# Performance work log

Measured on AMD Instinct MI355X. Metric: run time of the kernel, lower is better.

Reference implementation:

```python
import jax, jax.numpy as jnp
import numpy as np

B, LQ, D, DFF, NH, DH, NL, NP = 8, 1024, 256, 1024, 8, 32, 3, 4
_SHAPES = np.array([[100, 100], [50, 50], [25, 25]], dtype=np.int32)  # (H, W) per level
_AREAS = _SHAPES[:, 0] * _SHAPES[:, 1]
LIN = int(_AREAS.sum())  # 13125
_STARTS = np.concatenate([[0], np.cumsum(_AREAS)[:-1]]).astype(np.int32)


def setup_inputs() -> dict:
    key = jax.random.key(0)
    ks = iter(jax.random.split(key, 64))
    def rn(shape, s=1.0):
        return jax.random.normal(next(ks), shape, jnp.float32) * s
    return {
        "query_embed": rn((B, LQ, D)),
        "query_mask": jnp.zeros((B, LQ), bool),  # True = padded key
        "query_order": rn((B, LQ, D)),
        "values": rn((B, LIN, D)),
        "ref_point": jax.random.uniform(next(ks), (B, LQ, 2), jnp.float32),
        "ref_pos": rn((B, LQ, D)),
        "ref_feat": rn((B, LQ, D)),
        "shapes": jnp.asarray(_SHAPES),
        "level_start": jnp.asarray(_STARTS),
        "headwise_refpoint_idxs": jnp.zeros((B, LQ), jnp.int32),  # unused (side_head=0)
        # self-attention sub-block params (nn.MultiheadAttention packed in-proj)
        "sa_in_w": rn((D, 3 * D), 0.02), "sa_in_b": jnp.zeros((3 * D,)),
        "sa_out_w": rn((D, D), 0.02), "sa_out_b": jnp.zeros((D,)),
        "sa_ln1_g": jnp.ones((D,)), "sa_ln1_b": jnp.zeros((D,)),
        "sa_l1_w": rn((D, DFF), 0.02), "sa_l1_b": jnp.zeros((DFF,)),
        "sa_l2_w": rn((DFF, D), 0.02), "sa_l2_b": jnp.zeros((D,)),
        "sa_ln2_g": jnp.ones((D,)), "sa_ln2_b": jnp.zeros((D,)),
        # MDeformAttn params
        "da_val_w": rn((D, D), 0.02), "da_val_b": jnp.zeros((D,)),
        "da_off_w": rn((D, NH * NL * NP * 2), 0.001), "da_off_b": rn((NH * NL * NP * 2,), 0.01),
        "da_att_w": rn((D, NH * NL * NP), 0.02), "da_att_b": jnp.zeros((NH * NL * NP,)),
        "da_out_w": rn((D, D), 0.02), "da_out_b": jnp.zeros((D,)),
        # post-deform FFN block params
        "ln1_g": jnp.ones((D,)), "ln1_b": jnp.zeros((D,)),
        "ff1_w": rn((D, DFF), 0.02), "ff1_b": jnp.zeros((DFF,)),
        "ff2_w": rn((DFF, D), 0.02), "ff2_b": jnp.zeros((D,)),
        "ln2_g": jnp.ones((D,)), "ln2_b": jnp.zeros((D,)),
    }


def _ln(x, g, b):
    m = jnp.mean(x, -1, keepdims=True)
    v = jnp.mean((x - m) ** 2, -1, keepdims=True)
    return (x - m) / jnp.sqrt(v + 1e-5) * g + b


def _mha(q, k, v, key_padding_mask, in_w, in_b, out_w, out_b):
    Bv = q.shape[0]
    qp = (q @ in_w[:, :D] + in_b[:D]).reshape(Bv, -1, NH, DH)
    kp = (k @ in_w[:, D:2 * D] + in_b[D:2 * D]).reshape(Bv, -1, NH, DH)
    vp = (v @ in_w[:, 2 * D:] + in_b[2 * D:]).reshape(Bv, -1, NH, DH)
    scores = jnp.einsum('bqhd,bkhd->bhqk', qp, kp) / jnp.sqrt(jnp.float32(DH))
    scores = scores + jnp.where(key_padding_mask[:, None, None, :], -1e9, 0.0)
    a = jax.nn.softmax(scores, -1)
    o = jnp.einsum('bhqk,bkhd->bqhd', a, vp).reshape(Bv, -1, D)
    return o @ out_w + out_b


def _ms_deform(query, ref_point, values, shapes,
               val_w, val_b, off_w, off_b, att_w, att_b, out_w, out_b):
    # Multi-scale deformable attention (MDeformAttn, align_corners=False bilinear, zero pad)
    Bv, Lq = query.shape[0], query.shape[1]
    v = (values @ val_w + val_b).reshape(Bv, -1, NH, DH)
    off = (query @ off_w + off_b).reshape(Bv, Lq, NH, NL, NP, 2)
    attn = jax.nn.softmax((query @ att_w + att_b).reshape(Bv, Lq, NH, NL * NP), -1)
    attn = attn.reshape(Bv, Lq, NH, NL, NP)
    norm = jnp.stack([shapes[:, 1], shapes[:, 0]], -1).astype(jnp.float32)  # (W, H)
    loc = ref_point[:, :, None, None, None, :] + off / norm[None, None, None, :, None, :]
    acc = 0.0
    for lvl in range(NL):  # static spatial shapes per level
        Hl, Wl = int(_SHAPES[lvl, 0]), int(_SHAPES[lvl, 1])
        s = int(_STARTS[lvl])
        vl = v[:, s:s + Hl * Wl].transpose(0, 2, 1, 3)  # [B,NH,Hl*Wl,DH]
        ll = loc[:, :, :, lvl]                          # [B,Lq,NH,NP,2]
        x = ll[..., 0] * Wl - 0.5
        y = ll[..., 1] * Hl - 0.5
        x0 = jnp.floor(x); y0 = jnp.floor(y)
        wx = x - x0; wy = y - y0
        x0i = x0.astype(jnp.int32); y0i = y0.astype(jnp.int32)
        def tw(w):  # [B,Lq,NH,NP] -> [B,NH,Lq*NP,1]
            return w.transpose(0, 2, 1, 3).reshape(Bv, NH, -1, 1)
        def gather(yy, xx):
            valid = ((yy >= 0) & (yy < Hl) & (xx >= 0) & (xx < Wl))
            idx = jnp.clip(yy, 0, Hl - 1) * Wl + jnp.clip(xx, 0, Wl - 1)
            idx_t = idx.transpose(0, 2, 1, 3).reshape(Bv, NH, -1)
            g = jnp.take_along_axis(vl, idx_t[..., None], axis=2)  # [B,NH,Lq*NP,DH]
            return g * tw(valid.astype(vl.dtype))
        samp = (tw((1 - wy) * (1 - wx)) * gather(y0i, x0i)
                + tw((1 - wy) * wx) * gather(y0i, x0i + 1)
                + tw(wy * (1 - wx)) * gather(y0i + 1, x0i)
                + tw(wy * wx) * gather(y0i + 1, x0i + 1))
        aw = tw(attn[:, :, :, lvl])
        acc = acc + (samp * aw).reshape(Bv, NH, Lq, NP, DH).sum(3)
    out = acc.transpose(0, 2, 1, 3).reshape(Bv, Lq, D)
    return out @ out_w + out_b


def reference(query_embed, query_mask, query_order, values, ref_point, ref_pos, ref_feat,
              shapes, level_start, headwise_refpoint_idxs,
              sa_in_w, sa_in_b, sa_out_w, sa_out_b, sa_ln1_g, sa_ln1_b,
              sa_l1_w, sa_l1_b, sa_l2_w, sa_l2_b, sa_ln2_g, sa_ln2_b,
              da_val_w, da_val_b, da_off_w, da_off_b, da_att_w, da_att_b, da_out_w, da_out_b,
              ln1_g, ln1_b, ff1_w, ff1_b, ff2_w, ff2_b, ln2_g, ln2_b):
    # forward_self_att(tgt + ref_feat, query_order + ref_pos, query_mask); dropout = identity (eval)
    src = query_embed + ref_feat
    pos = query_order + ref_pos
    q = src + pos
    src = _ln(src + _mha(q, q, src, query_mask, sa_in_w, sa_in_b, sa_out_w, sa_out_b), sa_ln1_g, sa_ln1_b)
    src = _ln(src + (jax.nn.relu(src @ sa_l1_w + sa_l1_b) @ sa_l2_w + sa_l2_b), sa_ln2_g, sa_ln2_b)
    tgt = src
    dq = tgt + query_order + ref_pos + ref_feat
    tgt2 = _ms_deform(dq, ref_point, values, shapes,
                      da_val_w, da_val_b, da_off_w, da_off_b, da_att_w, da_att_b, da_out_w, da_out_b)
    tgt = _ln(tgt + tgt2, ln1_g, ln1_b)
    tgt = _ln(tgt + (jax.nn.relu(tgt @ ff1_w + ff1_b) @ ff2_w + ff2_b), ln2_g, ln2_b)
    return tgt
```

## Files before the change

### kernel.cpp

```cpp
#include <hip/hip_runtime.h>
#include <math.h>

#define B_   8
#define LQ_  1024
#define D_   256
#define NH_  8
#define DH_  32
#define LIN_ 13125

typedef __attribute__((ext_vector_type(4))) float f32x4;
typedef __attribute__((ext_vector_type(8))) short bf16x8;
typedef __attribute__((ext_vector_type(4))) short bf16x4;

__device__ __forceinline__ float4 f4add(float4 a, float4 b){
  return make_float4(a.x+b.x, a.y+b.y, a.z+b.z, a.w+b.w);
}
__device__ __forceinline__ unsigned short f2bf(float f){
  unsigned u = __float_as_uint(f);
  unsigned r = (u + 0x7fffu + ((u>>16)&1u)) >> 16;
  return (unsigned short)r;
}
__device__ __forceinline__ float bf2f(unsigned short u){
  return __uint_as_float(((unsigned)u)<<16);
}
__device__ __forceinline__ unsigned pk2(float a, float b){
  return (unsigned)f2bf(a) | ((unsigned)f2bf(b)<<16);
}
__device__ __forceinline__ float fexp2(float x){
#if __has_builtin(__builtin_amdgcn_exp2f)
  return __builtin_amdgcn_exp2f(x);
#else
  return exp2f(x);
#endif
}
__device__ __forceinline__ f32x4 mfma16x16(bf16x4 a, bf16x4 b, f32x4 c){
#if __has_builtin(__builtin_amdgcn_mfma_f32_16x16x16_bf16)
  return __builtin_amdgcn_mfma_f32_16x16x16_bf16(a, b, c, 0, 0, 0);
#else
  asm volatile("s_nop 1\n\tv_mfma_f32_16x16x16_bf16 %0, %1, %2, %0"
               : "+v"(c) : "v"(a), "v"(b));
  return c;
#endif
}
__device__ __forceinline__ void gload16(const void* g, void* l){
  __builtin_amdgcn_global_load_lds(
      (const __attribute__((address_space(1))) void*)g,
      (__attribute__((address_space(3))) void*)l, 16, 0, 0);
}
__device__ __forceinline__ bf16x8 cvt8(const float4& a, const float4& b){
  unsigned u0,u1,u2,u3;
  asm("v_cvt_pk_bf16_f32 %0, %1, %2" : "=v"(u0) : "v"(a.x), "v"(a.y));
  asm("v_cvt_pk_bf16_f32 %0, %1, %2" : "=v"(u1) : "v"(a.z), "v"(a.w));
  asm("v_cvt_pk_bf16_f32 %0, %1, %2" : "=v"(u2) : "v"(b.x), "v"(b.y));
  asm("v_cvt_pk_bf16_f32 %0, %1, %2" : "=v"(u3) : "v"(b.z), "v"(b.w));
  uint4 uu = make_uint4(u0,u1,u2,u3);
  return __builtin_bit_cast(bf16x8, uu);
}
__device__ __forceinline__ int xcd_swz(int lin, int nwg){
  if (nwg < 64) return lin;
  const int q = nwg >> 3, r = nwg & 7;
  const int x = lin & 7, d = lin >> 3;
  return (x < r ? x*(q+1) : r*(q+1) + (x-r)*q) + d;
}

__global__ __launch_bounds__(256) void k_prep(
    const float4* __restrict__ qe, const float4* __restrict__ rf,
    const float4* __restrict__ qo, const float4* __restrict__ rp,
    const unsigned char* __restrict__ mask,
    const float* __restrict__ off_b, const float* __restrict__ att_b,
    float4* __restrict__ src, uint2* __restrict__ srcb, uint2* __restrict__ qb,
    float* __restrict__ biasf, float* __restrict__ biasoa)
{
  int i = blockIdx.x*256 + threadIdx.x;
  if (i < B_*LQ_) biasf[i] = mask[i] ? -2.0e9f : 0.f;
  if (blockIdx.x == 32) {
    for (int j = threadIdx.x; j < 384; j += 256)
      biasoa[j] = (j < 192) ? off_b[j] : (j < 288 ? att_b[j-192] : 0.f);
  }
  float4 s = f4add(qe[i], rf[i]);
  src[i] = s;
  float4 q = f4add(s, f4add(qo[i], rp[i]));
  srcb[i] = make_uint2(pk2(s.x,s.y), pk2(s.z,s.w));
  qb[i]   = make_uint2(pk2(q.x,q.y), pk2(q.z,q.w));
}

struct WEnt { const float* s; unsigned short* d; int K; int N; };
struct WPack { WEnt e[10]; };
__global__ __launch_bounds__(256) void k_wtcvt(WPack p)
{
  __shared__ float sm[32][33];
  WEnt w = p.e[blockIdx.y];
  const int tk = w.K >> 5, tn = w.N >> 5;
  const int nt = tk * tn;
  const int r = threadIdx.x >> 5, c = threadIdx.x & 31;
  for (int tile = blockIdx.x; tile < nt; tile += gridDim.x) {
    const int ti = tile / tn, tj = tile % tn;
    #pragma unroll
    for (int rr = r; rr < 32; rr += 8)
      sm[rr][c] = w.s[(size_t)(ti*32+rr)*w.N + tj*32 + c];
    __syncthreads();
    #pragma unroll
    for (int rr = r; rr < 32; rr += 8)
      w.d[(size_t)(tj*32+rr)*w.K + ti*32 + c] = f2bf(sm[c][rr]);
    __syncthreads();
  }
}

template<bool BF16OUT>
__global__ __launch_bounds__(256) void k_gemm_bf(
    const unsigned short* __restrict__ A, int lda,
    const unsigned short* __restrict__ Wt,
    const float* __restrict__ bias,
    float* __restrict__ Cf, unsigned short* __restrict__ Cb, int ldc,
    int M, int N, int K, int relu)
{
  __shared__ unsigned short As[2][4096];
  __shared__ unsigned short Bs[2][4096];
  const int t = threadIdx.x;
  const int lin = xcd_swz(blockIdx.y*gridDim.x + blockIdx.x, gridDim.x*gridDim.y);
  const int bx = lin % gridDim.x, by = lin / gridDim.x;
  const int m0 = by * 128;
  const int n0 = bx * 128;
  const int w  = t >> 6, lane = t & 63;
  const int lr = lane & 15, lg = lane >> 4;
  const int wm = (w & 1) * 64, wn = (w >> 1) * 64;

  const int rowc  = t >> 2;
  const int cbs8  = (((t & 3) ^ ((t >> 2) & 3)) << 3);
  const size_t ra0 = (size_t)min(m0 + rowc,      M-1) * lda;
  const size_t ra1 = (size_t)min(m0 + rowc + 64, M-1) * lda;
  const size_t rb0 = (size_t)(n0 + rowc)      * K;
  const size_t rb1 = (size_t)(n0 + rowc + 64) * K;
  unsigned short* la0[2] = { &As[0][(w<<9)],        &As[1][(w<<9)] };
  unsigned short* la1[2] = { &As[0][2048+(w<<9)],   &As[1][2048+(w<<9)] };
  unsigned short* lb0[2] = { &Bs[0][(w<<9)],        &Bs[1][(w<<9)] };
  unsigned short* lb1[2] = { &Bs[0][2048+(w<<9)],   &Bs[1][2048+(w<<9)] };

  f32x4 acc[4][4];
  #pragma unroll
  for (int i=0;i<4;++i)
    #pragma unroll
    for (int j=0;j<4;++j) acc[i][j] = (f32x4){0.f,0.f,0.f,0.f};

  const int cswz = ((lg ^ (lr & 3)) << 3);
  const int nt = K >> 5;

  {
    gload16(A  + ra0 + cbs8, la0[0]);
    gload16(A  + ra1 + cbs8, la1[0]);
    gload16(Wt + rb0 + cbs8, lb0[0]);
    gload16(Wt + rb1 + cbs8, lb1[0]);
  }
  for (int ks = 0; ks < nt; ++ks) {
    const int cur = ks & 1;
    __syncthreads();
    if (ks + 1 < nt) {
      const int kb = (ks + 1) << 5;
      const int nb = cur ^ 1;
      gload16(A  + ra0 + kb + cbs8, la0[nb]);
      gload16(A  + ra1 + kb + cbs8, la1[nb]);
      gload16(Wt + rb0 + kb + cbs8, lb0[nb]);
      gload16(Wt + rb1 + kb + cbs8, lb1[nb]);
    }
    bf16x8 af[4], bfr[4];
    #pragma unroll
    for (int mi=0;mi<4;++mi)
      af[mi]  = *reinterpret_cast<const bf16x8*>(&As[cur][(wm+mi*16+lr)*32 + cswz]);
    #pragma unroll
    for (int ni=0;ni<4;++ni)
      bfr[ni] = *reinterpret_cast<const bf16x8*>(&Bs[cur][(wn+ni*16+lr)*32 + cswz]);
    #pragma unroll
    for (int mi=0;mi<4;++mi)
      #pragma unroll
      for (int ni=0;ni<4;++ni)
        acc[mi][ni] = __builtin_amdgcn_mfma_f32_16x16x32_bf16(af[mi], bfr[ni], acc[mi][ni], 0, 0, 0);
  }

  float bs[4];
  #pragma unroll
  for (int ni=0;ni<4;++ni) bs[ni] = bias[n0 + wn + ni*16 + lr];
  #pragma unroll
  for (int mi=0;mi<4;++mi){
    #pragma unroll
    for (int i=0;i<4;++i){
      const int row = m0 + wm + mi*16 + lg*4 + i;
      if (row >= M) continue;
      #pragma unroll
      for (int ni=0;ni<4;++ni){
        const int col = n0 + wn + ni*16 + lr;
        float v = acc[mi][ni][i] + bs[ni];
        if (relu) v = fmaxf(v, 0.f);
        if (BF16OUT) Cb[(size_t)row*ldc + col] = f2bf(v);
        else         Cf[(size_t)row*ldc + col] = v;
      }
    }
  }
}

__global__ __launch_bounds__(256, 2) void k_gemm_vp(
    const float* __restrict__ A,
    const unsigned short* __restrict__ Wt,
    const float* __restrict__ bias,
    unsigned short* __restrict__ Cb, int M)
{
  __shared__ unsigned short Ws[32768];
  const int t = threadIdx.x;
  const int lin = xcd_swz(blockIdx.y*gridDim.x + blockIdx.x, gridDim.x*gridDim.y);
  const int bx = lin % gridDim.x, by = lin / gridDim.x;
  const int n0 = bx * 128;
  const int m0 = by * 256;
  const int w = t >> 6, lane = t & 63;
  const int lr = lane & 15, lg = lane >> 4;

  #pragma unroll
  for (int q = 0; q < 16; ++q) {
    const int c = q*256 + t;
    const int row = c >> 5, pos = c & 31;
    gload16(Wt + (size_t)(n0 + row)*256 + ((pos ^ (row & 31)) << 3),
            (unsigned short*)Ws + (size_t)c*8);
  }
  __syncthreads();

  float bs[8];
  #pragma unroll
  for (int ni=0;ni<8;++ni) bs[ni] = bias[n0 + ni*16 + lr];

  const int mw = m0 + w*64;
  float4 avA[8][2], avB[8][2];
  #pragma unroll
  for (int kk=0;kk<8;++kk){
    const size_t ad = (size_t)min(mw + lr, M-1)*256 + kk*32 + lg*8;
    avA[kk][0] = *reinterpret_cast<const float4*>(A + ad);
    avA[kk][1] = *reinterpret_cast<const float4*>(A + ad + 4);
  }
  #pragma unroll
  for (int s = 0; s < 4; ++s) {
    const int mb = mw + s*16;
    if (s < 3) {
      #pragma unroll
      for (int kk=0;kk<8;++kk){
        const size_t ad = (size_t)min(mb + 16 + lr, M-1)*256 + kk*32 + lg*8;
        if (s & 1) {
          avA[kk][0] = *reinterpret_cast<const float4*>(A + ad);
          avA[kk][1] = *reinterpret_cast<const float4*>(A + ad + 4);
        } else {
          avB[kk][0] = *reinterpret_cast<const float4*>(A + ad);
          avB[kk][1] = *reinterpret_cast<const float4*>(A + ad + 4);
        }
      }
    }
    bf16x8 af[8];
    #pragma unroll
    for (int kk=0;kk<8;++kk)
      af[kk] = (s & 1) ? cvt8(avB[kk][0], avB[kk][1]) : cvt8(avA[kk][0], avA[kk][1]);
    f32x4 acc[8];
    #pragma unroll
    for (int ni=0;ni<8;++ni) acc[ni] = (f32x4){0.f,0.f,0.f,0.f};
    #pragma unroll
    for (int kk=0;kk<8;++kk){
      #pragma unroll
      for (int ni=0;ni<8;++ni){
        const int r = ni*16 + lr;
        const int p = (kk*4 + lg) ^ (r & 31);
        bf16x8 wf = *reinterpret_cast<const bf16x8*>(&Ws[r*256 + (p<<3)]);
        acc[ni] = __builtin_amdgcn_mfma_f32_16x16x32_bf16(af[kk], wf, acc[ni], 0, 0, 0);
      }
    }
    #pragma unroll
    for (int ni=0;ni<8;++ni){
      const int col = n0 + ni*16 + lr;
      #pragma unroll
      for (int i=0;i<4;++i){
        const int row = mb + lg*4 + i;
        if (row < M) Cb[(size_t)row*256 + col] = f2bf(acc[ni][i] + bs[ni]);
      }
    }
  }
}

template<int EPI>
__global__ __launch_bounds__(256) void k_gemm64(
    const unsigned short* __restrict__ A, int lda,
    const unsigned short* __restrict__ Wt,
    const float* __restrict__ bias,
    float* __restrict__ Cf, unsigned short* __restrict__ Cb, int ldc,
    int M, int N, int K, int relu)
{
  __shared__ unsigned short As[2][4096];
  __shared__ unsigned short Bs[2][4096];
  const int t = threadIdx.x;
  const int lin = xcd_swz(blockIdx.y*gridDim.x + blockIdx.x, gridDim.x*gridDim.y);
  const int bx = lin % gridDim.x, by = lin / gridDim.x;
  const int m0 = by * 64;
  const int n0 = bx * 64;
  const int w = t >> 6, lane = t & 63;
  const int lr = lane & 15, lg = lane >> 4;
  const int wm = (w & 1) * 32, wn = (w >> 1) * 32;

  const int c0 = w*64 + lane;
  const int c1 = 256 + w*64 + lane;
  const int r0c = c0 >> 3, s0c = ((c0 & 7) ^ (r0c & 7)) << 3;
  const int r1c = c1 >> 3, s1c = ((c1 & 7) ^ (r1c & 7)) << 3;
  const size_t a0 = (size_t)(m0 + r0c)*lda + s0c;
  const size_t a1 = (size_t)(m0 + r1c)*lda + s1c;
  const size_t b0 = (size_t)(n0 + r0c)*K + s0c;
  const size_t b1 = (size_t)(n0 + r1c)*K + s1c;
  const int d0 = w*512, d1 = 2048 + w*512;

  f32x4 acc[2][2];
  acc[0][0]=acc[0][1]=acc[1][0]=acc[1][1]=(f32x4){0.f,0.f,0.f,0.f};

  gload16(A + a0, &As[0][d0]);  gload16(A + a1, &As[0][d1]);
  gload16(Wt + b0, &Bs[0][d0]); gload16(Wt + b1, &Bs[0][d1]);
  const int nt = K >> 6;
  for (int ks = 0; ks < nt; ++ks) {
    const int cur = ks & 1;
    __syncthreads();
    if (ks + 1 < nt) {
      const int kb = (ks + 1) << 6;
      const int nb = cur ^ 1;
      gload16(A + kb + a0, &As[nb][d0]);  gload16(A + kb + a1, &As[nb][d1]);
      gload16(Wt + kb + b0, &Bs[nb][d0]); gload16(Wt + kb + b1, &Bs[nb][d1]);
    }
    bf16x8 af[2][2], bfr[2][2];
    #pragma unroll
    for (int mi=0;mi<2;++mi){
      const int r = wm + mi*16 + lr;
      #pragma unroll
      for (int kk=0;kk<2;++kk){
        const int ch = ((kk*4 + lg) ^ (r & 7)) << 3;
        af[mi][kk] = *reinterpret_cast<const bf16x8*>(&As[cur][r*64 + ch]);
      }
    }
    #pragma unroll
    for (int ni=0;ni<2;++ni){
      const int r = wn + ni*16 + lr;
      #pragma unroll
      for (int kk=0;kk<2;++kk){
        const int ch = ((kk*4 + lg) ^ (r & 7)) << 3;
        bfr[ni][kk] = *reinterpret_cast<const bf16x8*>(&Bs[cur][r*64 + ch]);
      }
    }
    #pragma unroll
    for (int kk=0;kk<2;++kk)
      #pragma unroll
      for (int mi=0;mi<2;++mi)
        #pragma unroll
        for (int ni=0;ni<2;++ni)
          acc[mi][ni] = __builtin_amdgcn_mfma_f32_16x16x32_bf16(af[mi][kk], bfr[ni][kk], acc[mi][ni], 0, 0, 0);
  }

  float bs[2];
  bs[0] = bias[n0 + wn + lr];
  bs[1] = bias[n0 + wn + 16 + lr];
  if (EPI == 3) {
    #pragma unroll
    for (int mi=0;mi<2;++mi){
      const int rowb = m0 + wm + mi*16 + lg*4;
      #pragma unroll
      for (int ni=0;ni<2;++ni){
        const int colb = n0 + wn + ni*16 + lr;
        const int bh = (rowb >> 10)*8 + (colb >> 5);
        const int d = colb & 31;
        ushort4 pkv;
        pkv.x = f2bf(acc[mi][ni][0] + bs[ni]);
        pkv.y = f2bf(acc[mi][ni][1] + bs[ni]);
        pkv.z = f2bf(acc[mi][ni][2] + bs[ni]);
        pkv.w = f2bf(acc[mi][ni][3] + bs[ni]);
        *reinterpret_cast<ushort4*>(Cb + (size_t)bh*32768 + (size_t)d*1024 + (rowb & 1023)) = pkv;
      }
    }
    return;
  }
  #pragma unroll
  for (int mi=0;mi<2;++mi){
    #pragma unroll
    for (int i=0;i<4;++i){
      const int row = m0 + wm + mi*16 + lg*4 + i;
      #pragma unroll
      for (int ni=0;ni<2;++ni){
        const int col = n0 + wn + ni*16 + lr;
        float v = acc[mi][ni][i] + bs[ni];
        if (relu) v = fmaxf(v, 0.f);
        if (EPI == 0) {
          Cf[(size_t)row*ldc + col] = v;
        } else if (EPI == 1) {
          Cb[(size_t)row*ldc + col] = f2bf(v);
        } else {
          const int ch = col & 255;
          const int sel = col >> 8;
          const int bh = (row >> 10)*8 + (ch >> 5);
          Cb[(size_t)sel*2097152 + (size_t)bh*32768 + (size_t)(row & 1023)*32 + (ch & 31)] = f2bf(v);
        }
      }
    }
  }
}

__global__ __launch_bounds__(256) void k_gemm_ln(
    const unsigned short* __restrict__ A, int lda,
    const unsigned short* __restrict__ Wt,
    const float* __restrict__ bias,
    const float* __restrict__ X,
    const float* __restrict__ g, const float* __restrict__ be,
    float* __restrict__ out,
    unsigned short* __restrict__ ab,
    const float* __restrict__ qo, const float* __restrict__ rp,
    const float* __restrict__ rf, unsigned short* __restrict__ dqb,
    int K)
{
  __shared__ unsigned short As[2][1024];
  __shared__ unsigned short Bs[2][16384];
  __shared__ float part[4][16][2];
  const int t = threadIdx.x;
  const int w = t >> 6, lane = t & 63;
  const int lr = lane & 15, lg = lane >> 4;
  const int m0 = xcd_swz(blockIdx.x, gridDim.x) * 16;

  const int ar = t >> 3, ac = t & 7;
  const size_t aSrc = (size_t)(m0 + ar)*lda + ((ac ^ (ar & 7)) << 3);
  size_t bSrc[8];
  #pragma unroll
  for (int q=0;q<8;++q){
    const int c = q*256 + t;
    const int br = c >> 3, bc = c & 7;
    bSrc[q] = (size_t)br*K + ((bc ^ (br & 7)) << 3);
  }

  f32x4 acc[4];
  #pragma unroll
  for (int ni=0;ni<4;++ni) acc[ni] = (f32x4){0.f,0.f,0.f,0.f};

  if (w < 2) gload16(A + aSrc, &As[0][(w<<9)]);
  #pragma unroll
  for (int q=0;q<8;++q) gload16(Wt + bSrc[q], &Bs[0][q*2048 + (w<<9)]);

  const int nt = K >> 6;
  for (int ks = 0; ks < nt; ++ks) {
    const int cur = ks & 1;
    __syncthreads();
    if (ks + 1 < nt) {
      const int kb = (ks + 1) << 6;
      const int nb = cur ^ 1;
      if (w < 2) gload16(A + kb + aSrc, &As[nb][(w<<9)]);
      #pragma unroll
      for (int q=0;q<8;++q) gload16(Wt + kb + bSrc[q], &Bs[nb][q*2048 + (w<<9)]);
    }
    bf16x8 af[2];
    #pragma unroll
    for (int kk=0;kk<2;++kk){
      const int ch = ((kk*4 + lg) ^ (lr & 7)) << 3;
      af[kk] = *reinterpret_cast<const bf16x8*>(&As[cur][lr*64 + ch]);
    }
    #pragma unroll
    for (int ni=0;ni<4;++ni){
      const int r = w*64 + ni*16 + lr;
      #pragma unroll
      for (int kk=0;kk<2;++kk){
        const int ch = ((kk*4 + lg) ^ (r & 7)) << 3;
        bf16x8 bfv = *reinterpret_cast<const bf16x8*>(&Bs[cur][r*64 + ch]);
        acc[ni] = __builtin_amdgcn_mfma_f32_16x16x32_bf16(af[kk], bfv, acc[ni], 0, 0, 0);
      }
    }
  }

  float v[4][4];
  int colv[4];
  #pragma unroll
  for (int ni=0;ni<4;++ni) colv[ni] = w*64 + ni*16 + lr;
  #pragma unroll
  for (int ni=0;ni<4;++ni){
    const float bsv = bias[colv[ni]];
    #pragma unroll
    for (int i=0;i<4;++i){
      const int row = m0 + lg*4 + i;
      v[ni][i] = acc[ni][i] + bsv + X[(size_t)row*256 + colv[ni]];
    }
  }
  #pragma unroll
  for (int i=0;i<4;++i){
    float s1 = v[0][i]+v[1][i]+v[2][i]+v[3][i];
    float s2 = v[0][i]*v[0][i]+v[1][i]*v[1][i]+v[2][i]*v[2][i]+v[3][i]*v[3][i];
    #pragma unroll
    for (int o=1;o<16;o<<=1){ s1 += __shfl_xor(s1,o,64); s2 += __shfl_xor(s2,o,64); }
    if (lr == 0){ part[w][lg*4+i][0] = s1; part[w][lg*4+i][1] = s2; }
  }
  __syncthreads();
  #pragma unroll
  for (int i=0;i<4;++i){
    const int rl = lg*4 + i;
    const float S1 = part[0][rl][0]+part[1][rl][0]+part[2][rl][0]+part[3][rl][0];
    const float S2 = part[0][rl][1]+part[1][rl][1]+part[2][rl][1]+part[3][rl][1];
    const float mean = S1 * 0.00390625f;
    const float var  = S2 * 0.00390625f - mean*mean;
    const float rstd = rsqrtf(var + 1e-5f);
    const size_t row = m0 + rl;
    #pragma unroll
    for (int ni=0;ni<4;++ni){
      const int col = colv[ni];
      const float o = (v[ni][i]-mean)*rstd*g[col] + be[col];
      out[row*256 + col] = o;
      if (ab) ab[row*256 + col] = f2bf(o);
      if (dqb) {
        const float e = qo[row*256+col] + rp[row*256+col] + rf[row*256+col];
        dqb[row*256 + col] = f2bf(o + e);
      }
    }
  }
}

__global__ __launch_bounds__(256) void k_attn2(
    const unsigned short* __restrict__ Qbf,
    const unsigned short* __restrict__ Kbf,
    const unsigned short* __restrict__ Vtb,
    const float* __restrict__ biasf,
    unsigned short* __restrict__ Ob)
{
  __shared__ unsigned short Klds[2][2048];
  __shared__ unsigned short Vlds[2][2048];
  __shared__ float Blds[1024];
  const int t = threadIdx.x;
  const int wv = t >> 6, lane = t & 63;
  const int lin = xcd_swz(blockIdx.y*gridDim.x + blockIdx.x, gridDim.x*gridDim.y);
  const int bx = lin % gridDim.x, by = lin / gridDim.x;
  const int qt = bx * 4 + wv;
  const int bh = by;
  const int b = bh >> 3;
  const int q0 = qt << 4;
  const int lr = lane & 15, lg = lane >> 4;

  bf16x8 qf = *reinterpret_cast<const bf16x8*>(
      Qbf + (size_t)bh*32768 + (size_t)(q0 + lr)*32 + lg*8);

  *reinterpret_cast<float4*>(&Blds[t*4]) =
      *reinterpret_cast<const float4*>(biasf + b*1024 + t*4);

  const unsigned short* Kg = Kbf + (size_t)bh*32768;
  const unsigned short* Vg = Vtb + (size_t)bh*32768;

  const int kRow   = lane >> 2;
  const int kChunk = (lane & 3) ^ (kRow & 3);
  const size_t kSrc = (size_t)(wv*16 + kRow)*32 + (kChunk<<3);
  const int vDim   = lane >> 3;
  const int vChunk = (lane & 7) ^ vDim;
  const size_t vSrc = (size_t)(wv*8 + vDim)*1024 + (vChunk<<3);
  unsigned short* kDst[2] = { &Klds[0][wv<<9], &Klds[1][wv<<9] };
  unsigned short* vDst[2] = { &Vlds[0][wv<<9], &Vlds[1][wv<<9] };

  gload16(Kg + kSrc, kDst[0]);
  gload16(Vg + vSrc, vDst[0]);
  __syncthreads();

  f32x4 acc0 = {0.f,0.f,0.f,0.f}, acc1 = {0.f,0.f,0.f,0.f};
  float m_run = -1e30f, l_run = 0.f;
  const float Cs = 0.17677669529663687f * 1.4426950408889634f;
  const int kswz = (lg ^ (lr & 3)) << 3;

  for (int kt = 0; kt < 16; ++kt) {
    const int cur = kt & 1;
    if (kt + 1 < 16) {
      const size_t k0n = (size_t)(kt + 1) << 6;
      gload16(Kg + k0n*32 + kSrc, kDst[cur^1]);
      gload16(Vg + k0n    + vSrc, vDst[cur^1]);
    }
    f32x4 st[4];
    __builtin_amdgcn_s_setprio(1);
    #pragma unroll
    for (int j=0;j<4;++j){
      bf16x8 kf = *reinterpret_cast<const bf16x8*>(&Klds[cur][(16*j + lr)*32 + kswz]);
      f32x4 z = {0.f,0.f,0.f,0.f};
      st[j] = __builtin_amdgcn_mfma_f32_16x16x32_bf16(kf, qf, z, 0, 0, 0);
    }
    __builtin_amdgcn_s_setprio(0);
    const int k0 = kt << 6;
    float s[16];
    #pragma unroll
    for (int j=0;j<4;++j){
      float4 bv = *reinterpret_cast<const float4*>(&Blds[k0 + 16*j + lg*4]);
      s[4*j+0] = fmaf(st[j][0], Cs, bv.x);
      s[4*j+1] = fmaf(st[j][1], Cs, bv.y);
      s[4*j+2] = fmaf(st[j][2], Cs, bv.z);
      s[4*j+3] = fmaf(st[j][3], Cs, bv.w);
    }
    float mc = fmaxf(fmaxf(fmaxf(s[0],s[1]),fmaxf(s[2],s[3])),
                     fmaxf(fmaxf(s[4],s[5]),fmaxf(s[6],s[7])));
    float mc2 = fmaxf(fmaxf(fmaxf(s[8],s[9]),fmaxf(s[10],s[11])),
                      fmaxf(fmaxf(s[12],s[13]),fmaxf(s[14],s[15])));
    mc = fmaxf(mc, mc2);
    mc = fmaxf(mc, __shfl_xor(mc, 16, 64));
    mc = fmaxf(mc, __shfl_xor(mc, 32, 64));
    if (!__all(mc <= m_run + 8.f)) {
      float m_new = fmaxf(m_run, mc);
      float sc = fexp2(m_run - m_new);
      l_run *= sc;
      m_run = m_new;
      float sc0 = __shfl(sc, lg*4+0, 64);
      float sc1 = __shfl(sc, lg*4+1, 64);
      float sc2 = __shfl(sc, lg*4+2, 64);
      float sc3 = __shfl(sc, lg*4+3, 64);
      acc0[0]*=sc0; acc0[1]*=sc1; acc0[2]*=sc2; acc0[3]*=sc3;
      acc1[0]*=sc0; acc1[1]*=sc1; acc1[2]*=sc2; acc1[3]*=sc3;
    }
    float p[16];
    #pragma unroll
    for (int i=0;i<16;++i) p[i] = fexp2(s[i] - m_run);
    float ps = 0.f;
    #pragma unroll
    for (int i=0;i<16;++i) ps += p[i];
    ps += __shfl_xor(ps, 16, 64);
    ps += __shfl_xor(ps, 32, 64);
    l_run += ps;
    bf16x4 pb[4];
    #pragma unroll
    for (int j=0;j<4;++j){
      unsigned lo, hi;
      asm("v_cvt_pk_bf16_f32 %0, %1, %2" : "=v"(lo) : "v"(p[4*j+0]), "v"(p[4*j+1]));
      asm("v_cvt_pk_bf16_f32 %0, %1, %2" : "=v"(hi) : "v"(p[4*j+2]), "v"(p[4*j+3]));
      uint2 u = make_uint2(lo, hi);
      pb[j] = __builtin_bit_cast(bf16x4, u);
    }
    __builtin_amdgcn_s_setprio(1);
    #pragma unroll
    for (int j=0;j<4;++j){
      const int coff = (((2*j + (lg>>1)) ^ (lr & 7)) << 3) + ((lg & 1) << 2);
      bf16x4 v0 = *reinterpret_cast<const bf16x4*>(&Vlds[cur][lr*64 + coff]);
      bf16x4 v1 = *reinterpret_cast<const bf16x4*>(&Vlds[cur][(16+lr)*64 + coff]);
      acc0 = mfma16x16(pb[j], v0, acc0);
      acc1 = mfma16x16(pb[j], v1, acc1);
    }
    __builtin_amdgcn_s_setprio(0);
    __syncthreads();
  }
  float li[4];
  #pragma unroll
  for (int i=0;i<4;++i) li[i] = 1.f / __shfl(l_run, lg*4+i, 64);
  const int h = bh & 7;
  unsigned short* orow = Ob + (size_t)(b*1024 + q0)*256 + h*32;
  #pragma unroll
  for (int i=0;i<4;++i){
    orow[(size_t)(lg*4+i)*256 + lr]      = f2bf(acc0[i]*li[i]);
    orow[(size_t)(lg*4+i)*256 + 16 + lr] = f2bf(acc1[i]*li[i]);
  }
}

__global__ __launch_bounds__(256) void k_dgather2(
    const unsigned short* __restrict__ vproj,
    const float* __restrict__ IJ,
    const float* __restrict__ refp,
    unsigned short* __restrict__ outb)
{
  __shared__ int   ilds[8][12][4];
  __shared__ float wlds[8][12][4];
  const int t = threadIdx.x;
  const int bq = blockIdx.x;
  const int h = t >> 5;
  const int p = t & 31;
  if (p < 12) {
    const float* al = IJ + (size_t)bq*384 + 192 + h*12;
    float lg[12];
    float mx = -INFINITY;
    #pragma unroll
    for (int i=0;i<12;++i){ lg[i] = al[i]; mx = fmaxf(mx, lg[i]); }
    float se = 0.f;
    #pragma unroll
    for (int i=0;i<12;++i) se += __expf(lg[i]-mx);
    const float aw = __expf(lg[p]-mx) / se;
    const float rx = refp[(size_t)bq*2+0], ry = refp[(size_t)bq*2+1];
    const float ox = IJ[(size_t)bq*384 + h*24 + 2*p];
    const float oy = IJ[(size_t)bq*384 + h*24 + 2*p + 1];
    const int l = p >> 2;
    const int WW[3]={100,50,25}, SS[3]={0,10000,12500};
    const int Wi = WW[l], Hi = WW[l], s0 = SS[l];
    const float Wf = (float)Wi, Hf = (float)Hi;
    const float x = (rx + ox/Wf)*Wf - 0.5f;
    const float y = (ry + oy/Hf)*Hf - 0.5f;
    const float x0f = floorf(x), y0f = floorf(y);
    const float wx = x - x0f, wy = y - y0f;
    const int x0 = (int)x0f, y0 = (int)y0f;
    const int xs0 = min(max(x0,0),Wi-1),   xs1 = min(max(x0+1,0),Wi-1);
    const int ys0 = min(max(y0,0),Hi-1),   ys1 = min(max(y0+1,0),Hi-1);
    const bool vx0 = (x0>=0)&&(x0<Wi),     vx1 = (x0+1>=0)&&(x0+1<Wi);
    const bool vy0 = (y0>=0)&&(y0<Hi),     vy1 = (y0+1>=0)&&(y0+1<Hi);
    const int vb = (bq >> 10) * LIN_;
    ilds[h][p][0] = vb + s0 + ys0*Wi + xs0;
    ilds[h][p][1] = vb + s0 + ys0*Wi + xs1;
    ilds[h][p][2] = vb + s0 + ys1*Wi + xs0;
    ilds[h][p][3] = vb + s0 + ys1*Wi + xs1;
    wlds[h][p][0] = (vy0&&vx0)? (1.f-wy)*(1.f-wx)*aw : 0.f;
    wlds[h][p][1] = (vy0&&vx1)? (1.f-wy)*wx*aw       : 0.f;
    wlds[h][p][2] = (vy1&&vx0)? wy*(1.f-wx)*aw       : 0.f;
    wlds[h][p][3] = (vy1&&vx1)? wy*wx*aw             : 0.f;
  }
  __syncthreads();
  const int col = t;
  float acc = 0.f;
  #pragma unroll
  for (int pt=0; pt<12; ++pt){
    acc = fmaf(wlds[h][pt][0], bf2f(vproj[(size_t)ilds[h][pt][0]*256 + col]), acc);
    acc = fmaf(wlds[h][pt][1], bf2f(vproj[(size_t)ilds[h][pt][1]*256 + col]), acc);
    acc = fmaf(wlds[h][pt][2], bf2f(vproj[(size_t)ilds[h][pt][2]*256 + col]), acc);
    acc = fmaf(wlds[h][pt][3], bf2f(vproj[(size_t)ilds[h][pt][3]*256 + col]), acc);
  }
  outb[(size_t)bq*256 + col] = f2bf(acc);
}

extern "C" void kernel_launch(void* const* d_in, const int* in_sizes, int n_in,
                              void* d_out, int out_size, void* d_ws, size_t ws_size,
                              hipStream_t stream)
{
  const float* qe      = (const float*)d_in[0];
  const unsigned char* qmask = (const unsigned char*)d_in[1];
  const float* qo      = (const float*)d_in[2];
  const float* values  = (const float*)d_in[3];
  const float* refp    = (const float*)d_in[4];
  const float* rp      = (const float*)d_in[5];
  const float* rf      = (const float*)d_in[6];
  const float* sa_in_w = (const float*)d_in[10];
  const float* sa_in_b = (const float*)d_in[11];
  const float* sa_out_w= (const float*)d_in[12];
  const float* sa_out_b= (const float*)d_in[13];
  const float* sa_ln1_g= (const float*)d_in[14];
  const float* sa_ln1_b= (const float*)d_in[15];
  const float* sa_l1_w = (const float*)d_in[16];
  const float* sa_l1_b = (const float*)d_in[17];
  const float* sa_l2_w = (const float*)d_in[18];
  const float* sa_l2_b = (const float*)d_in[19];
  const float* sa_ln2_g= (const float*)d_in[20];
  const float* sa_ln2_b= (const float*)d_in[21];
  const float* da_val_w= (const float*)d_in[22];
  const float* da_val_b= (const float*)d_in[23];
  const float* da_off_w= (const float*)d_in[24];
  const float* da_off_b= (const float*)d_in[25];
  const float* da_att_w= (const float*)d_in[26];
  const float* da_att_b= (const float*)d_in[27];
  const float* da_out_w= (const float*)d_in[28];
  const float* da_out_b= (const float*)d_in[29];
  const float* ln1_g   = (const float*)d_in[30];
  const float* ln1_b   = (const float*)d_in[31];
  const float* ff1_w   = (const float*)d_in[32];
  const float* ff1_b   = (const float*)d_in[33];
  const float* ff2_w   = (const float*)d_in[34];
  const float* ff2_b   = (const float*)d_in[35];
  const float* ln2_g   = (const float*)d_in[36];
  const float* ln2_b   = (const float*)d_in[37];

  float* Wk = (float*)d_ws;
  const size_t MEG = 1u<<20;
  float* A   = Wk;
  unsigned short* Ab   = (unsigned short*)(Wk + 4*MEG);
  unsigned short* hidb = (unsigned short*)(Wk + 5*MEG);
  unsigned short* WT   = (unsigned short*)(Wk + 9*MEG);
  unsigned short* qb   = (unsigned short*)(Wk + 10*MEG);
  unsigned short* srcb = (unsigned short*)(Wk + 11*MEG);
  unsigned short* Qbf  = (unsigned short*)(Wk + 12*MEG);
  unsigned short* Kbf  = (unsigned short*)(Wk + 13*MEG);
  unsigned short* Vtb  = (unsigned short*)(Wk + 15*MEG);
  unsigned short* aob  = (unsigned short*)(Wk + 16*MEG);
  unsigned short* dqb  = (unsigned short*)(Wk + 10*MEG);
  float* IJ = Wk + 12*MEG;
  unsigned short* Hb = (unsigned short*)(Wk + 37*MEG);
  unsigned short* dG = (unsigned short*)(Wk + 51*MEG);
  float* biasf  = Wk + 52*MEG;
  float* biasoa = Wk + 52*MEG + 8192;

  unsigned short* sa_inT  = WT;
  unsigned short* sa_outT = WT + 196608;
  unsigned short* sa_l1T  = WT + 262144;
  unsigned short* sa_l2T  = WT + 524288;
  unsigned short* da_valT = WT + 786432;
  unsigned short* da_outT = WT + 851968;
  unsigned short* ff1T    = WT + 917504;
  unsigned short* ff2T    = WT + 1179648;
  unsigned short* offattT = WT + 1441792;

  WPack wp_;
  wp_.e[0] = { sa_in_w, sa_inT, 256, 768 };
  wp_.e[1] = { sa_out_w, sa_outT, 256, 256 };
  wp_.e[2] = { sa_l1_w, sa_l1T, 256, 1024 };
  wp_.e[3] = { sa_l2_w, sa_l2T, 1024, 256 };
  wp_.e[4] = { da_val_w, da_valT, 256, 256 };
  wp_.e[5] = { da_out_w, da_outT, 256, 256 };
  wp_.e[6] = { ff1_w, ff1T, 256, 1024 };
  wp_.e[7] = { ff2_w, ff2T, 1024, 256 };
  wp_.e[8] = { da_off_w, offattT, 256, 192 };
  wp_.e[9] = { da_att_w, offattT + 192*256, 256, 96 };

  dim3 blk(256);
  k_wtcvt<<<dim3(64,10), blk, 0, stream>>>(wp_);
  k_prep<<<2048, blk, 0, stream>>>((const float4*)qe,(const float4*)rf,
                                   (const float4*)qo,(const float4*)rp,
                                   qmask, da_off_b, da_att_b,
                                   (float4*)A,(uint2*)srcb,(uint2*)qb,
                                   biasf, biasoa);
  k_gemm64<2><<<dim3(8,128), blk, 0, stream>>>(qb,256, sa_inT, sa_in_b, nullptr,Qbf,0, 8192,512,256, 0);
  k_gemm64<3><<<dim3(4,128), blk, 0, stream>>>(srcb,256, sa_inT+512*256, sa_in_b+512, nullptr,Vtb,0, 8192,256,256, 0);
  k_attn2<<<dim3(16,64), blk, 0, stream>>>(Qbf, Kbf, Vtb, biasf, aob);
  k_gemm_ln<<<512, blk, 0, stream>>>(aob,256, sa_outT, sa_out_b, A,
                                     sa_ln1_g, sa_ln1_b, A, Ab,
                                     nullptr, nullptr, nullptr, nullptr, 256);
  k_gemm_bf<true><<<dim3(8,64), blk, 0, stream>>>(Ab,256, sa_l1T, sa_l1_b, nullptr,hidb,1024, 8192,1024,256, 1);
  k_gemm_ln<<<512, blk, 0, stream>>>(hidb,1024, sa_l2T, sa_l2_b, A,
                                     sa_ln2_g, sa_ln2_b, A, Ab,
                                     qo, rp, rf, dqb, 1024);
  k_gemm64<0><<<dim3(6,128), blk, 0, stream>>>(dqb,256, offattT, biasoa, IJ,nullptr,384, 8192,384,256, 0);
  k_gemm_vp<<<dim3(2,411), blk, 0, stream>>>(values, da_valT, da_val_b, Hb, 105000);
  k_dgather2<<<8192, blk, 0, stream>>>(Hb, IJ, refp, dG);
  k_gemm_ln<<<512, blk, 0, stream>>>(dG,256, da_outT, da_out_b, A,
                                     ln1_g, ln1_b, A, Ab,
                                     nullptr, nullptr, nullptr, nullptr, 256);
  k_gemm_bf<true><<<dim3(8,64), blk, 0, stream>>>(Ab,256, ff1T, ff1_b, nullptr,hidb,1024, 8192,1024,256, 1);
  k_gemm_ln<<<512, blk, 0, stream>>>(hidb,1024, ff2T, ff2_b, A,
                                     ln2_g, ln2_b, (float*)d_out, nullptr,
                                     nullptr, nullptr, nullptr, nullptr, 1024);
}
```

Before: 235.7 us.

## Hold value-projection weight fragments in registers instead of LDS

The value-projection GEMM stops staging the 128-column weight tile in shared memory. Each wave now loads its own 64-column by 256-K weight fragments straight into registers, then walks 128 rows in 16-row steps with single-buffered prefetch of the fp32 activations. This removes the 64KB LDS footprint and the per-MFMA LDS reads, and drops the 2-blocks-per-CU launch bound. In exchange it raises VGPR pressure (32 bf16x8 weight fragments per lane), which may lower occupancy, and it reads weights redundantly from global memory.

```diff
diff --git a/kernel.cpp b/kernel.cpp
--- a/kernel.cpp
+++ b/kernel.cpp
@@ -197,78 +197,66 @@
   }
 }
 
-__global__ __launch_bounds__(256, 2) void k_gemm_vp(
+__global__ __launch_bounds__(256) void k_gemm_vp(
     const float* __restrict__ A,
     const unsigned short* __restrict__ Wt,
     const float* __restrict__ bias,
     unsigned short* __restrict__ Cb, int M)
 {
-  __shared__ unsigned short Ws[32768];
   const int t = threadIdx.x;
   const int lin = xcd_swz(blockIdx.y*gridDim.x + blockIdx.x, gridDim.x*gridDim.y);
   const int bx = lin % gridDim.x, by = lin / gridDim.x;
-  const int n0 = bx * 128;
-  const int m0 = by * 256;
   const int w = t >> 6, lane = t & 63;
   const int lr = lane & 15, lg = lane >> 4;
-
-  #pragma unroll
-  for (int q = 0; q < 16; ++q) {
-    const int c = q*256 + t;
-    const int row = c >> 5, pos = c & 31;
-    gload16(Wt + (size_t)(n0 + row)*256 + ((pos ^ (row & 31)) << 3),
-            (unsigned short*)Ws + (size_t)c*8);
-  }
-  __syncthreads();
-
-  float bs[8];
-  #pragma unroll
-  for (int ni=0;ni<8;++ni) bs[ni] = bias[n0 + ni*16 + lr];
-
-  const int mw = m0 + w*64;
-  float4 avA[8][2], avB[8][2];
-  #pragma unroll
-  for (int kk=0;kk<8;++kk){
-    const size_t ad = (size_t)min(mw + lr, M-1)*256 + kk*32 + lg*8;
-    avA[kk][0] = *reinterpret_cast<const float4*>(A + ad);
-    avA[kk][1] = *reinterpret_cast<const float4*>(A + ad + 4);
-  }
-  #pragma unroll
-  for (int s = 0; s < 4; ++s) {
-    const int mb = mw + s*16;
-    if (s < 3) {
+  const int cw  = bx * 128 + (w & 1) * 64;
+  const int mwv = by * 256 + (w >> 1) * 128;
+
+  bf16x8 wf[8][4];
+  #pragma unroll
+  for (int kk=0;kk<8;++kk)
+    #pragma unroll
+    for (int ni=0;ni<4;++ni)
+      wf[kk][ni] = *reinterpret_cast<const bf16x8*>(
+          Wt + (size_t)(cw + ni*16 + lr)*256 + kk*32 + lg*8);
+
+  float bs[4];
+  #pragma unroll
+  for (int ni=0;ni<4;++ni) bs[ni] = bias[cw + ni*16 + lr];
+
+  float4 av[8][2];
+  {
+    const size_t r0 = (size_t)min(mwv + lr, M-1)*256;
+    #pragma unroll
+    for (int kk=0;kk<8;++kk){
+      av[kk][0] = *reinterpret_cast<const float4*>(A + r0 + kk*32 + lg*8);
+      av[kk][1] = *reinterpret_cast<const float4*>(A + r0 + kk*32 + lg*8 + 4);
+    }
+  }
+  #pragma unroll
+  for (int s = 0; s < 8; ++s) {
+    const int mb = mwv + s*16;
+    bf16x8 af[8];
+    #pragma unroll
+    for (int kk=0;kk<8;++kk) af[kk] = cvt8(av[kk][0], av[kk][1]);
+    if (s < 7) {
+      const size_t rn = (size_t)min(mb + 16 + lr, M-1)*256;
       #pragma unroll
       for (int kk=0;kk<8;++kk){
-        const size_t ad = (size_t)min(mb + 16 + lr, M-1)*256 + kk*32 + lg*8;
-        if (s & 1) {
-          avA[kk][0] = *reinterpret_cast<const float4*>(A + ad);
-          avA[kk][1] = *reinterpret_cast<const float4*>(A + ad + 4);
-        } else {
-          avB[kk][0] = *reinterpret_cast<const float4*>(A + ad);
-          avB[kk][1] = *reinterpret_cast<const float4*>(A + ad + 4);
-        }
+        av[kk][0] = *reinterpret_cast<const float4*>(A + rn + kk*32 + lg*8);
+        av[kk][1] = *reinterpret_cast<const float4*>(A + rn + kk*32 + lg*8 + 4);
       }
     }
-    bf16x8 af[8];
+    f32x4 acc[4];
+    #pragma unroll
+    for (int ni=0;ni<4;++ni) acc[ni] = (f32x4){0.f,0.f,0.f,0.f};
     #pragma unroll
     for (int kk=0;kk<8;++kk)
-      af[kk] = (s & 1) ? cvt8(avB[kk][0], avB[kk][1]) : cvt8(avA[kk][0], avA[kk][1]);
-    f32x4 acc[8];
-    #pragma unroll
-    for (int ni=0;ni<8;++ni) acc[ni] = (f32x4){0.f,0.f,0.f,0.f};
-    #pragma unroll
-    for (int kk=0;kk<8;++kk){
-      #pragma unroll
-      for (int ni=0;ni<8;++ni){
-        const int r = ni*16 + lr;
-        const int p = (kk*4 + lg) ^ (r & 31);
-        bf16x8 wf = *reinterpret_cast<const bf16x8*>(&Ws[r*256 + (p<<3)]);
-        acc[ni] = __builtin_amdgcn_mfma_f32_16x16x32_bf16(af[kk], wf, acc[ni], 0, 0, 0);
-      }
-    }
-    #pragma unroll
-    for (int ni=0;ni<8;++ni){
-      const int col = n0 + ni*16 + lr;
+      #pragma unroll
+      for (int ni=0;ni<4;++ni)
+        acc[ni] = __builtin_amdgcn_mfma_f32_16x16x32_bf16(af[kk], wf[kk][ni], acc[ni], 0, 0, 0);
+    #pragma unroll
+    for (int ni=0;ni<4;++ni){
+      const int col = cw + ni*16 + lr;
       #pragma unroll
       for (int i=0;i<4;++i){
         const int row = mb + lg*4 + i;
```

Result: slower. 263.5 us (+11.8%).
